# Kernel optimization log

Hardware: AMD Instinct MI355X
Metric: run time of the kernel (lower is better)

The kernel has to match this reference:

```python
import jax, jax.numpy as jnp
import numpy as np
import math

B, T, D, H, E, K = 2, 1024, 1024, 2048, 8, 2
CAP_FRAC = 0.25


def setup_inputs() -> dict:
    key = jax.random.key(0)
    ks = jax.random.split(key, 6)
    s = 0.02  # weight scale (orig uses TruncatedNormal; scale kept sane)
    return {
        "x": jax.random.normal(ks[0], (B, T, D), dtype=jnp.float32),
        "router_w": jax.random.normal(ks[1], (D, E), dtype=jnp.float32) * s,
        "router_b": jax.random.normal(ks[2], (E,), dtype=jnp.float32) * s,
        "w1": jax.random.normal(ks[3], (E, D, H), dtype=jnp.float32) * s,
        "w2": jax.random.normal(ks[4], (E, D, H), dtype=jnp.float32) * s,
        "w3": jax.random.normal(ks[5], (E, H, D), dtype=jnp.float32) * s,
    }


def reference(x, router_w, router_b, w1, w2, w3):
    b, t, d = x.shape
    Bt = b * t
    cap = math.floor(Bt * CAP_FRAC)  # expert capacity C (static)
    x_flat = x.reshape(Bt, d)

    # ---- router: fp32 scores, top-k, softmax over selected experts ----
    scores = x_flat.astype(jnp.float32) @ router_w + router_b  # (Bt, E)
    top_scores, assign = jax.lax.top_k(scores, K)               # (Bt, K)
    gates = jax.nn.softmax(top_scores, axis=-1).astype(x.dtype)

    # ---- capacity-based token->expert assignment via one-hot cumsum ----
    onehot = jax.nn.one_hot(assign, E)                          # (Bt, K, E)
    pos = jnp.cumsum(jnp.cumsum(onehot, axis=0), axis=1).astype(jnp.int32)
    mask = onehot * jnp.less(pos, cap)                          # (Bt, K, E)
    token_mask = jnp.sum(mask, axis=-1)                         # (Bt, K)
    # dispatch tensor: (E, C, Bt)
    choices = jnp.sum(jax.nn.one_hot(pos, cap) * mask[..., None], axis=1)
    choices = choices.transpose(1, 2, 0).astype(jnp.int32)
    e_id = jnp.einsum('tke,e->tk', mask, jnp.arange(E, dtype=mask.dtype)).astype(jnp.int32)
    p_id = jnp.einsum('tke,tke->tk', mask, pos.astype(mask.dtype)).astype(jnp.int32)

    # ---- dispatch ----
    grouped = jnp.einsum('ect,td->ecd', choices.astype(x.dtype), x_flat)  # (E, C, D)

    # ---- grouped expert FFN: gelu(w2(x) * w1(x)) @ w3 ----
    h = jnp.einsum('ecd,edh->ech', grouped, w2) * jnp.einsum('ecd,edh->ech', grouped, w1)
    h = jax.nn.gelu(h)
    eo = jnp.einsum('ech,ehd->ecd', h, w3)                      # (E, C, D)

    # ---- combine ----
    e_id = e_id.reshape(b, t, K)
    p_id = p_id.reshape(b, t, K)
    token_mask = token_mask.reshape(b, t, K)
    gates = gates.reshape(b, t, K)
    out = eo[e_id, p_id]                                        # (b, t, K, D)
    out = jnp.where(token_mask[..., None].astype(bool), out, x[..., None, :])
    return jnp.einsum('btkd,btk->btd', out, gates)
```

## Files before the change

kernel.cpp:

```cpp
#include <hip/hip_runtime.h>
#include <hip/hip_bf16.h>
#include <math.h>

#define BT   2048
#define DD   1024
#define HH   2048
#define EE   8
#define CAP  512

typedef unsigned short u16;
typedef unsigned int   u32;
typedef short bf16x8 __attribute__((ext_vector_type(8)));
typedef float f32x4  __attribute__((ext_vector_type(4)));
typedef u16   u16x4  __attribute__((ext_vector_type(4)));

#define AS1 __attribute__((address_space(1)))
#define AS3 __attribute__((address_space(3)))

__device__ __forceinline__ u16 f2bf(float f) {
    union { float f; u32 u; } v; v.f = f;
    return (u16)((v.u + 0x7fffu + ((v.u >> 16) & 1u)) >> 16);
}
__device__ __forceinline__ float bf2f(u16 b) {
    union { u32 u; float f; } v; v.u = ((u32)b) << 16;
    return v.f;
}
__device__ __forceinline__ u32 pkbf(float lo, float hi) {
    u32 r;
    asm("v_cvt_pk_bf16_f32 %0, %1, %2" : "=v"(r) : "v"(lo), "v"(hi));
    return r;
}

__global__ __launch_bounds__(256) void router_kernel(
    const float* __restrict__ x, const float* __restrict__ rw,
    const float* __restrict__ rb, int2* __restrict__ assign,
    float2* __restrict__ gates)
{
    int t   = blockIdx.x;
    int tid = threadIdx.x;
    const float* xr = x + (size_t)t * DD;

    float p[EE];
    #pragma unroll
    for (int e = 0; e < EE; ++e) p[e] = 0.f;

    for (int d = tid; d < DD; d += 256) {
        float xv = xr[d];
        const float4* wr = (const float4*)(rw + (size_t)d * EE);
        float4 w0 = wr[0], w1 = wr[1];
        p[0] += xv * w0.x; p[1] += xv * w0.y; p[2] += xv * w0.z; p[3] += xv * w0.w;
        p[4] += xv * w1.x; p[5] += xv * w1.y; p[6] += xv * w1.z; p[7] += xv * w1.w;
    }
    #pragma unroll
    for (int off = 32; off; off >>= 1) {
        #pragma unroll
        for (int e = 0; e < EE; ++e) p[e] += __shfl_down(p[e], off);
    }
    __shared__ float red[4][EE];
    int wv = tid >> 6, ln = tid & 63;
    if (ln == 0) {
        #pragma unroll
        for (int e = 0; e < EE; ++e) red[wv][e] = p[e];
    }
    __syncthreads();
    if (tid == 0) {
        float s[EE];
        #pragma unroll
        for (int e = 0; e < EE; ++e)
            s[e] = red[0][e] + red[1][e] + red[2][e] + red[3][e] + rb[e];
        int i0 = 0;
        #pragma unroll
        for (int e = 1; e < EE; ++e) if (s[e] > s[i0]) i0 = e;
        int i1 = -1;
        #pragma unroll
        for (int e = 0; e < EE; ++e) {
            if (e == i0) continue;
            if (i1 < 0 || s[e] > s[i1]) i1 = e;
        }
        float e1 = expf(s[i1] - s[i0]);
        float denom = 1.0f + e1;
        assign[t] = make_int2(i0, i1);
        gates[t]  = make_float2(1.0f / denom, e1 / denom);
    }
}

__global__ __launch_bounds__(64) void scan_kernel(
    const int2* __restrict__ assign, int4* __restrict__ meta,
    int2* __restrict__ slot_tok)
{
    __shared__ int c0[64][EE];
    __shared__ int cA[64][EE];
    int l = threadIdx.x;

    for (int i = l; i < EE * CAP; i += 64) slot_tok[i] = make_int2(-1, -1);
    #pragma unroll
    for (int e = 0; e < EE; ++e) { c0[l][e] = 0; cA[l][e] = 0; }
    __syncthreads();

    const int CH = BT / 64;
    int t0 = l * CH;

    for (int t = t0; t < t0 + CH; ++t) {
        int2 a = assign[t];
        c0[l][a.x]++; cA[l][a.x]++; cA[l][a.y]++;
    }
    __syncthreads();

    #pragma unroll
    for (int e = 0; e < EE; ++e) {
        int v = c0[l][e], inc = v;
        for (int d = 1; d < 64; d <<= 1) { int u = __shfl_up(inc, d); if (l >= d) inc += u; }
        c0[l][e] = inc - v;
        v = cA[l][e]; inc = v;
        for (int d = 1; d < 64; d <<= 1) { int u = __shfl_up(inc, d); if (l >= d) inc += u; }
        cA[l][e] = inc - v;
    }
    __syncthreads();

    for (int t = t0; t < t0 + CH; ++t) {
        int2 a = assign[t];
        int p0 = ++c0[l][a.x];  cA[l][a.x]++;
        int p1 = ++cA[l][a.y];
        int4 m;
        m.x = a.x; m.y = (p0 < CAP) ? p0 : -1;
        m.z = a.y; m.w = (p1 < CAP) ? p1 : -1;
        meta[t] = m;
        int* st = (int*)slot_tok;
        if (p0 < CAP) st[(a.x * CAP + p0) * 2 + 0] = t;
        if (p1 < CAP) st[(a.y * CAP + p1) * 2 + 1] = t;
    }
}

__global__ __launch_bounds__(256) void gather_bf16(
    const float* __restrict__ x, const int2* __restrict__ slot_tok,
    u16* __restrict__ G)
{
    int es = blockIdx.x;
    int d  = threadIdx.x * 4;
    int2 st = slot_tok[es];
    float4 r = make_float4(0.f, 0.f, 0.f, 0.f);
    if (st.x >= 0) r = *(const float4*)(x + (size_t)st.x * DD + d);
    if (st.y >= 0) {
        float4 v = *(const float4*)(x + (size_t)st.y * DD + d);
        r.x += v.x; r.y += v.y; r.z += v.z; r.w += v.w;
    }
    u16x4 o;
    o[0] = f2bf(r.x); o[1] = f2bf(r.y); o[2] = f2bf(r.z); o[3] = f2bf(r.w);
    *(u16x4*)(G + (size_t)es * DD + d) = o;
}


__global__ __launch_bounds__(512, 4) void gemm1_mfma(
    const u16* __restrict__ G, const float* __restrict__ W1,
    const float* __restrict__ W2, u16* __restrict__ H)
{
    __shared__ u16   As [256 * 32];
    __shared__ float B1s[32 * 64];
    __shared__ float B2s[32 * 64];

    const int e  = blockIdx.z;
    const int n0 = blockIdx.x * 64;
    const int m0 = blockIdx.y * 256;
    const int tid  = threadIdx.x;
    const int lane = tid & 63;
    const int w    = tid >> 6;
    const int wr = w >> 2, wc = w & 3;
    const int lr = lane & 15, lq = lane >> 4;

    const char* Ab  = (const char*)(G + (size_t)e * CAP * DD + (size_t)m0 * DD);
    const char* W1b = (const char*)(W1 + (size_t)e * DD * HH + n0);
    const char* W2b = (const char*)(W2 + (size_t)e * DD * HH + n0);

    const int srow = lane >> 2;
    const int skb  = ((lane & 3) ^ ((lane >> 3) & 3)) * 16;
    const int bkrow = w * 4 + (lane >> 4);
    const int bscc  = ((lane & 15) ^ ((5 * (w >> 1)) & 15)) * 16;

    f32x4 acc1[8] = {};
    f32x4 acc2[8] = {};

    for (int k0 = 0; k0 < DD; k0 += 32) {
        {
            const size_t kbyte = (size_t)k0 * 2 + skb;
            #pragma unroll
            for (int c2 = 0; c2 < 2; ++c2) {
                const int c = 2 * w + c2;
                const size_t rb = (size_t)(c * 16 + srow) * (DD * 2) + kbyte;
                __builtin_amdgcn_global_load_lds((const AS1 void*)(Ab + rb),
                    (AS3 void*)((char*)As + c * 1024), 16, 0, 0);
            }
        }
        {
            const size_t sb = (size_t)(k0 + bkrow) * (HH * 4) + bscc;
            __builtin_amdgcn_global_load_lds((const AS1 void*)(W1b + sb),
                (AS3 void*)((char*)B1s + w * 1024), 16, 0, 0);
            __builtin_amdgcn_global_load_lds((const AS1 void*)(W2b + sb),
                (AS3 void*)((char*)B2s + w * 1024), 16, 0, 0);
        }
        __syncthreads();
        bf16x8 av[8];
        #pragma unroll
        for (int m = 0; m < 8; ++m) {
            const int row = wr * 128 + m * 16 + lr;
            const int sl  = (lq ^ ((row >> 1) & 3)) * 16;
            av[m] = *(const bf16x8*)((const char*)As + row * 64 + sl);
        }
        {
            const int n  = wc * 16 + lr;
            const int cb = ((((n >> 2) ^ (5 * lq)) & 15) << 4) + (n & 3) * 4;
            union { u32 q[4]; bf16x8 v; } u1, u2;
            #pragma unroll
            for (int i = 0; i < 4; ++i) {
                int o = (lq * 8 + 2 * i) * 256 + cb;
                asm("" : "+v"(o));
                u1.q[i] = pkbf(*(const float*)((const char*)B1s + o),
                               *(const float*)((const char*)B1s + o + 256));
                u2.q[i] = pkbf(*(const float*)((const char*)B2s + o),
                               *(const float*)((const char*)B2s + o + 256));
            }
            const bf16x8 b1 = u1.v, b2 = u2.v;
            #pragma unroll
            for (int m = 0; m < 8; ++m) {
                acc1[m] = __builtin_amdgcn_mfma_f32_16x16x32_bf16(av[m], b1, acc1[m], 0, 0, 0);
                acc2[m] = __builtin_amdgcn_mfma_f32_16x16x32_bf16(av[m], b2, acc2[m], 0, 0, 0);
            }
        }
        __syncthreads();
    }

    u16* He = H + (size_t)e * CAP * HH;
    const float gc0 = 0.7978845608028654f, gc1 = 0.044715f;
    const int cc = n0 + wc * 16 + lr;
    #pragma unroll
    for (int m = 0; m < 8; ++m)
        #pragma unroll
        for (int r = 0; r < 4; ++r) {
            const int rr = m0 + wr * 128 + m * 16 + lq * 4 + r;
            float hv = acc1[m][r] * acc2[m][r];
            float u  = gc0 * (hv + gc1 * hv * hv * hv);
            float th = 1.f - 2.f / (__expf(2.f * u) + 1.f);
            He[(size_t)rr * HH + cc] = f2bf(0.5f * hv * (1.f + th));
        }
}

__global__ __launch_bounds__(256, 2) void gemm2_mfma(
    const u16* __restrict__ Hin, const float* __restrict__ W3, u16* __restrict__ EO)
{
    __shared__ u16   As[128 * 32];
    __shared__ float Bs[32 * 128];

    const int e  = blockIdx.z;
    const int n0 = blockIdx.x * 128;
    const int m0 = blockIdx.y * 128;
    const int tid  = threadIdx.x;
    const int lane = tid & 63;
    const int w    = tid >> 6;
    const int lr = lane & 15, lq = lane >> 4;

    const char* Ab  = (const char*)(Hin + (size_t)e * CAP * HH + (size_t)m0 * HH);
    const char* W3b = (const char*)(W3 + (size_t)e * HH * DD + n0);

    const int srow = lane >> 2;
    const int skb  = ((lane & 3) ^ ((lane >> 3) & 3)) * 16;
    const int brow = lane >> 5;
    const int bso  = ((lane & 31) ^ ((w & 3) << 2)) * 16;

    f32x4 acc[8][2] = {};

    for (int k0 = 0; k0 < HH; k0 += 32) {
        {
            const size_t kbyte = (size_t)k0 * 2 + skb;
            #pragma unroll
            for (int c2 = 0; c2 < 2; ++c2) {
                const int c = 2 * w + c2;
                const size_t rb = (size_t)(c * 16 + srow) * (HH * 2) + kbyte;
                __builtin_amdgcn_global_load_lds((const AS1 void*)(Ab + rb),
                    (AS3 void*)((char*)As + c * 1024), 16, 0, 0);
            }
        }
        #pragma unroll
        for (int i = 0; i < 4; ++i) {
            const int krow = w * 8 + i * 2 + brow;
            const size_t sb = (size_t)(k0 + krow) * (DD * 4) + bso;
            char* d3 = (char*)Bs + (w * 8 + i * 2) * 512;
            __builtin_amdgcn_global_load_lds((const AS1 void*)(W3b + sb),
                (AS3 void*)d3, 16, 0, 0);
        }
        __syncthreads();
        bf16x8 av[8];
        #pragma unroll
        for (int m = 0; m < 8; ++m) {
            const int row = m * 16 + lr;
            const int sl  = (lq ^ ((row >> 1) & 3)) * 16;
            av[m] = *(const bf16x8*)((const char*)As + row * 64 + sl);
        }
        #pragma unroll
        for (int nf = 0; nf < 2; ++nf) {
            const int col = (w * 32 + nf * 16 + lr) ^ (lq << 4);
            const int cb  = (lq * 1024 + col) * 4;
            union { u32 q[4]; bf16x8 v; } u3;
            #pragma unroll
            for (int i = 0; i < 4; ++i) {
                int o = cb + i * 1024;
                asm("" : "+v"(o));
                u3.q[i] = pkbf(*(const float*)((const char*)Bs + o),
                               *(const float*)((const char*)Bs + o + 512));
            }
            const bf16x8 b3 = u3.v;
            #pragma unroll
            for (int m = 0; m < 8; ++m)
                acc[m][nf] = __builtin_amdgcn_mfma_f32_16x16x32_bf16(av[m], b3, acc[m][nf], 0, 0, 0);
        }
        __syncthreads();
    }

    u16* Oe = EO + (size_t)e * CAP * DD;
    #pragma unroll
    for (int m = 0; m < 8; ++m)
        #pragma unroll
        for (int nf = 0; nf < 2; ++nf) {
            const int cc = n0 + w * 32 + nf * 16 + lr;
            #pragma unroll
            for (int r = 0; r < 4; ++r) {
                const int rr = m0 + m * 16 + lq * 4 + r;
                Oe[(size_t)rr * DD + cc] = f2bf(acc[m][nf][r]);
            }
        }
}

__global__ __launch_bounds__(256) void combine_kernel(
    const float* __restrict__ x, const u16* __restrict__ EO,
    const int4* __restrict__ meta, const float2* __restrict__ gates,
    float* __restrict__ out)
{
    int t = blockIdx.x;
    int d = threadIdx.x * 4;
    int4  m = meta[t];
    float2 g = gates[t];
    float4 xv = *(const float4*)(x + (size_t)t * DD + d);
    float4 v0 = xv, v1 = xv;
    if (m.y >= 0) {
        u16x4 q = *(const u16x4*)(EO + ((size_t)m.x * CAP + m.y) * DD + d);
        v0 = make_float4(bf2f(q[0]), bf2f(q[1]), bf2f(q[2]), bf2f(q[3]));
    }
    if (m.w >= 0) {
        u16x4 q = *(const u16x4*)(EO + ((size_t)m.z * CAP + m.w) * DD + d);
        v1 = make_float4(bf2f(q[0]), bf2f(q[1]), bf2f(q[2]), bf2f(q[3]));
    }
    float4 r;
    r.x = g.x * v0.x + g.y * v1.x;
    r.y = g.x * v0.y + g.y * v1.y;
    r.z = g.x * v0.z + g.y * v1.z;
    r.w = g.x * v0.w + g.y * v1.w;
    *(float4*)(out + (size_t)t * DD + d) = r;
}

extern "C" void kernel_launch(void* const* d_in, const int* in_sizes, int n_in,
                              void* d_out, int out_size, void* d_ws, size_t ws_size,
                              hipStream_t stream)
{
    const float* x  = (const float*)d_in[0];
    const float* rw = (const float*)d_in[1];
    const float* rb = (const float*)d_in[2];
    const float* w1 = (const float*)d_in[3];
    const float* w2 = (const float*)d_in[4];
    const float* w3 = (const float*)d_in[5];
    float* out = (float*)d_out;

    char* ws = (char*)d_ws;
    size_t off = 0;
    auto alloc = [&](size_t bytes) { char* p = ws + off; off = (off + bytes + 255) & ~(size_t)255; return p; };

    int2*   assign   = (int2*)  alloc(BT * sizeof(int2));
    float2* gates    = (float2*)alloc(BT * sizeof(float2));
    int4*   meta     = (int4*)  alloc(BT * sizeof(int4));
    int2*   slot_tok = (int2*)  alloc(EE * CAP * sizeof(int2));
    u16*    grouped  = (u16*)   alloc((size_t)EE * CAP * DD * 2);
    u16*    Hbuf     = (u16*)   alloc((size_t)EE * CAP * HH * 2);
    u16*    eo       = (u16*)   alloc((size_t)EE * CAP * DD * 2);
    (void)ws_size;

    router_kernel<<<BT, 256, 0, stream>>>(x, rw, rb, assign, gates);
    scan_kernel<<<1, 64, 0, stream>>>(assign, meta, slot_tok);
    gather_bf16<<<EE * CAP, 256, 0, stream>>>(x, slot_tok, grouped);

    gemm1_mfma<<<dim3(HH / 64, CAP / 256, EE), 512, 0, stream>>>(grouped, w1, w2, Hbuf);
    gemm2_mfma<<<dim3(DD / 128, CAP / 128, EE), 256, 0, stream>>>(Hbuf, w3, eo);

    combine_kernel<<<BT, 256, 0, stream>>>(x, eo, meta, gates, out);
}
```

Before: 145.2 us.

## Double K-step per barrier in both expert GEMMs and narrow gemm2 N tile

Both MFMA GEMMs now stage a 64-wide K slice per iteration instead of 32, so each pair of __syncthreads covers twice the MFMA work, with new LDS layouts and swizzles to match. gemm2's N tile drops from 128 to 64 columns per block, doubling its grid and halving per-wave accumulators. The aim is to cut barrier and loop overhead and raise occupancy in gemm2. In exchange LDS use per block grows and gemm2 reuses each loaded A tile across fewer output columns.

```diff
diff --git a/kernel.cpp b/kernel.cpp
--- a/kernel.cpp
+++ b/kernel.cpp
@@ -154,9 +154,9 @@
     const u16* __restrict__ G, const float* __restrict__ W1,
     const float* __restrict__ W2, u16* __restrict__ H)
 {
-    __shared__ u16   As [256 * 32];
-    __shared__ float B1s[32 * 64];
-    __shared__ float B2s[32 * 64];
+    __shared__ u16   As [256 * 64];
+    __shared__ float B1s[64 * 64];
+    __shared__ float B2s[64 * 64];
 
     const int e  = blockIdx.z;
     const int n0 = blockIdx.x * 64;
@@ -173,45 +173,48 @@
 
     const int srow = lane >> 2;
     const int skb  = ((lane & 3) ^ ((lane >> 3) & 3)) * 16;
-    const int bkrow = w * 4 + (lane >> 4);
-    const int bscc  = ((lane & 15) ^ ((5 * (w >> 1)) & 15)) * 16;
+    const int brow_i = lane >> 4;
+    const int bscc   = ((lane & 15) ^ ((5 * w) & 15)) * 16;
 
     f32x4 acc1[8] = {};
     f32x4 acc2[8] = {};
 
-    for (int k0 = 0; k0 < DD; k0 += 32) {
-        {
-            const size_t kbyte = (size_t)k0 * 2 + skb;
-            #pragma unroll
-            for (int c2 = 0; c2 < 2; ++c2) {
-                const int c = 2 * w + c2;
-                const size_t rb = (size_t)(c * 16 + srow) * (DD * 2) + kbyte;
-                __builtin_amdgcn_global_load_lds((const AS1 void*)(Ab + rb),
-                    (AS3 void*)((char*)As + c * 1024), 16, 0, 0);
-            }
-        }
-        {
-            const size_t sb = (size_t)(k0 + bkrow) * (HH * 4) + bscc;
+    for (int k0 = 0; k0 < DD; k0 += 64) {
+        #pragma unroll
+        for (int j = 0; j < 4; ++j) {
+            const int idx = 4 * w + j;
+            const int h = idx >> 4, c = idx & 15;
+            const size_t rb = (size_t)(c * 16 + srow) * (DD * 2)
+                            + (size_t)k0 * 2 + h * 64 + skb;
+            __builtin_amdgcn_global_load_lds((const AS1 void*)(Ab + rb),
+                (AS3 void*)((char*)As + idx * 1024), 16, 0, 0);
+        }
+        #pragma unroll
+        for (int i = 0; i < 2; ++i) {
+            const int krow = w * 8 + i * 4 + brow_i;
+            const size_t sb = (size_t)(k0 + krow) * (HH * 4) + bscc;
             __builtin_amdgcn_global_load_lds((const AS1 void*)(W1b + sb),
-                (AS3 void*)((char*)B1s + w * 1024), 16, 0, 0);
+                (AS3 void*)((char*)B1s + w * 2048 + i * 1024), 16, 0, 0);
             __builtin_amdgcn_global_load_lds((const AS1 void*)(W2b + sb),
-                (AS3 void*)((char*)B2s + w * 1024), 16, 0, 0);
+                (AS3 void*)((char*)B2s + w * 2048 + i * 1024), 16, 0, 0);
         }
         __syncthreads();
-        bf16x8 av[8];
-        #pragma unroll
-        for (int m = 0; m < 8; ++m) {
-            const int row = wr * 128 + m * 16 + lr;
-            const int sl  = (lq ^ ((row >> 1) & 3)) * 16;
-            av[m] = *(const bf16x8*)((const char*)As + row * 64 + sl);
-        }
-        {
-            const int n  = wc * 16 + lr;
-            const int cb = ((((n >> 2) ^ (5 * lq)) & 15) << 4) + (n & 3) * 4;
+        #pragma unroll
+        for (int h = 0; h < 2; ++h) {
+            bf16x8 av[8];
+            #pragma unroll
+            for (int m = 0; m < 8; ++m) {
+                const int row = wr * 128 + m * 16 + lr;
+                const int sl  = (lq ^ ((row >> 1) & 3)) * 16;
+                av[m] = *(const bf16x8*)((const char*)As + h * 16384 + row * 64 + sl);
+            }
+            const int n   = wc * 16 + lr;
+            const int lqh = h * 4 + lq;
+            const int cb  = ((((n >> 2) ^ (5 * lqh)) & 15) << 4) + (n & 3) * 4;
             union { u32 q[4]; bf16x8 v; } u1, u2;
             #pragma unroll
             for (int i = 0; i < 4; ++i) {
-                int o = (lq * 8 + 2 * i) * 256 + cb;
+                int o = (lqh * 8 + 2 * i) * 256 + cb;
                 asm("" : "+v"(o));
                 u1.q[i] = pkbf(*(const float*)((const char*)B1s + o),
                                *(const float*)((const char*)B1s + o + 256));
@@ -246,11 +249,11 @@
 __global__ __launch_bounds__(256, 2) void gemm2_mfma(
     const u16* __restrict__ Hin, const float* __restrict__ W3, u16* __restrict__ EO)
 {
-    __shared__ u16   As[128 * 32];
-    __shared__ float Bs[32 * 128];
+    __shared__ u16   As[128 * 64];
+    __shared__ float Bs[64 * 64];
 
     const int e  = blockIdx.z;
-    const int n0 = blockIdx.x * 128;
+    const int n0 = blockIdx.x * 64;
     const int m0 = blockIdx.y * 128;
     const int tid  = threadIdx.x;
     const int lane = tid & 63;
@@ -262,69 +265,65 @@
 
     const int srow = lane >> 2;
     const int skb  = ((lane & 3) ^ ((lane >> 3) & 3)) * 16;
-    const int brow = lane >> 5;
-    const int bso  = ((lane & 31) ^ ((w & 3) << 2)) * 16;
-
-    f32x4 acc[8][2] = {};
-
-    for (int k0 = 0; k0 < HH; k0 += 32) {
-        {
-            const size_t kbyte = (size_t)k0 * 2 + skb;
-            #pragma unroll
-            for (int c2 = 0; c2 < 2; ++c2) {
-                const int c = 2 * w + c2;
-                const size_t rb = (size_t)(c * 16 + srow) * (HH * 2) + kbyte;
-                __builtin_amdgcn_global_load_lds((const AS1 void*)(Ab + rb),
-                    (AS3 void*)((char*)As + c * 1024), 16, 0, 0);
-            }
+    const int brow_i = lane >> 4;
+
+    f32x4 acc[8] = {};
+
+    for (int k0 = 0; k0 < HH; k0 += 64) {
+        #pragma unroll
+        for (int j = 0; j < 4; ++j) {
+            const int idx = 4 * w + j;
+            const int h = idx >> 3, c = idx & 7;
+            const size_t rb = (size_t)(c * 16 + srow) * (HH * 2)
+                            + (size_t)k0 * 2 + h * 64 + skb;
+            __builtin_amdgcn_global_load_lds((const AS1 void*)(Ab + rb),
+                (AS3 void*)((char*)As + idx * 1024), 16, 0, 0);
         }
         #pragma unroll
         for (int i = 0; i < 4; ++i) {
-            const int krow = w * 8 + i * 2 + brow;
-            const size_t sb = (size_t)(k0 + krow) * (DD * 4) + bso;
-            char* d3 = (char*)Bs + (w * 8 + i * 2) * 512;
+            const int krow = w * 16 + i * 4 + brow_i;
+            const int bscc = ((lane & 15) ^ ((5 * (2 * w + (i >> 1))) & 15)) * 16;
+            const size_t sb = (size_t)(k0 + krow) * (DD * 4) + bscc;
             __builtin_amdgcn_global_load_lds((const AS1 void*)(W3b + sb),
-                (AS3 void*)d3, 16, 0, 0);
+                (AS3 void*)((char*)Bs + w * 4096 + i * 1024), 16, 0, 0);
         }
         __syncthreads();
-        bf16x8 av[8];
-        #pragma unroll
-        for (int m = 0; m < 8; ++m) {
-            const int row = m * 16 + lr;
-            const int sl  = (lq ^ ((row >> 1) & 3)) * 16;
-            av[m] = *(const bf16x8*)((const char*)As + row * 64 + sl);
-        }
-        #pragma unroll
-        for (int nf = 0; nf < 2; ++nf) {
-            const int col = (w * 32 + nf * 16 + lr) ^ (lq << 4);
-            const int cb  = (lq * 1024 + col) * 4;
+        #pragma unroll
+        for (int h = 0; h < 2; ++h) {
+            bf16x8 av[8];
+            #pragma unroll
+            for (int m = 0; m < 8; ++m) {
+                const int row = m * 16 + lr;
+                const int sl  = (lq ^ ((row >> 1) & 3)) * 16;
+                av[m] = *(const bf16x8*)((const char*)As + h * 8192 + row * 64 + sl);
+            }
+            const int n   = w * 16 + lr;
+            const int lqh = h * 4 + lq;
+            const int cb  = ((((n >> 2) ^ (5 * lqh)) & 15) << 4) + (n & 3) * 4;
             union { u32 q[4]; bf16x8 v; } u3;
             #pragma unroll
             for (int i = 0; i < 4; ++i) {
-                int o = cb + i * 1024;
+                int o = (lqh * 8 + 2 * i) * 256 + cb;
                 asm("" : "+v"(o));
                 u3.q[i] = pkbf(*(const float*)((const char*)Bs + o),
-                               *(const float*)((const char*)Bs + o + 512));
+                               *(const float*)((const char*)Bs + o + 256));
             }
             const bf16x8 b3 = u3.v;
             #pragma unroll
             for (int m = 0; m < 8; ++m)
-                acc[m][nf] = __builtin_amdgcn_mfma_f32_16x16x32_bf16(av[m], b3, acc[m][nf], 0, 0, 0);
+                acc[m] = __builtin_amdgcn_mfma_f32_16x16x32_bf16(av[m], b3, acc[m], 0, 0, 0);
         }
         __syncthreads();
     }
 
     u16* Oe = EO + (size_t)e * CAP * DD;
+    const int cc = n0 + w * 16 + lr;
     #pragma unroll
     for (int m = 0; m < 8; ++m)
         #pragma unroll
-        for (int nf = 0; nf < 2; ++nf) {
-            const int cc = n0 + w * 32 + nf * 16 + lr;
-            #pragma unroll
-            for (int r = 0; r < 4; ++r) {
-                const int rr = m0 + m * 16 + lq * 4 + r;
-                Oe[(size_t)rr * DD + cc] = f2bf(acc[m][nf][r]);
-            }
+        for (int r = 0; r < 4; ++r) {
+            const int rr = m0 + m * 16 + lq * 4 + r;
+            Oe[(size_t)rr * DD + cc] = f2bf(acc[m][r]);
         }
 }
 
@@ -385,7 +384,7 @@
     gather_bf16<<<EE * CAP, 256, 0, stream>>>(x, slot_tok, grouped);
 
     gemm1_mfma<<<dim3(HH / 64, CAP / 256, EE), 512, 0, stream>>>(grouped, w1, w2, Hbuf);
-    gemm2_mfma<<<dim3(DD / 128, CAP / 128, EE), 256, 0, stream>>>(Hbuf, w3, eo);
+    gemm2_mfma<<<dim3(DD / 64, CAP / 128, EE), 256, 0, stream>>>(Hbuf, w3, eo);
 
     combine_kernel<<<BT, 256, 0, stream>>>(x, eo, meta, gates, out);
 }
```

Result: faster. 123.7 us (-14.8%).
